# Performance work log

Hardware: AMD Instinct MI355X
Metric: run time of the kernel (lower is better)

Reference implementation:

```python
import jax, jax.numpy as jnp
import numpy as np

B, S, H, M, E = 64, 512, 1024, 26, 676  # batch, seq, hidden, max_nodes, max_edges (M*M)


def setup_inputs() -> dict:
    key = jax.random.key(0)
    ks = jax.random.split(key, 16)
    seq = jax.random.normal(ks[0], (B, S, H), jnp.float32)
    # ragged, strictly-increasing sentence-end offsets in [1, S-1], zero-padded tail
    rng = np.random.RandomState(0)
    off = np.zeros((B, M - 1), np.int64)
    for b in range(B):
        c = rng.randint(5, M)  # count of valid offsets per sample (ragged)
        off[b, :c] = np.sort(rng.choice(np.arange(1, S), size=c, replace=False))
    s = 1.0 / np.sqrt(H)
    s3 = 1.0 / np.sqrt(3 * H)
    return {
        'sequence_outputs': seq,
        'proof_offsets': jnp.asarray(off),
        'node_labels': jax.random.randint(ks[1], (B, M), 0, 2),
        'edge_labels': jax.random.randint(ks[2], (B, E), 0, 2),
        'W_naf': jax.random.normal(ks[3], (H, H), jnp.float32) * s,
        'b_naf': jnp.zeros((H,), jnp.float32),
        'W_cd': jax.random.normal(ks[4], (H, H), jnp.float32) * s,
        'b_cd': jnp.zeros((H,), jnp.float32),
        'W_co': jax.random.normal(ks[5], (H, 2), jnp.float32) * s,
        'b_co': jnp.zeros((2,), jnp.float32),
        'W_nd': jax.random.normal(ks[6], (H, H), jnp.float32) * s,
        'b_nd': jnp.zeros((H,), jnp.float32),
        'W_no': jax.random.normal(ks[7], (H, 2), jnp.float32) * s,
        'b_no': jnp.zeros((2,), jnp.float32),
        'W_ed': jax.random.normal(ks[8], (3 * H, H), jnp.float32) * s3,
        'b_ed': jnp.zeros((H,), jnp.float32),
        'W_eo': jax.random.normal(ks[9], (H, 2), jnp.float32) * s,
        'b_eo': jnp.zeros((2,), jnp.float32),
    }


def reference(sequence_outputs, proof_offsets, node_labels, edge_labels,
              W_naf, b_naf, W_cd, b_cd, W_co, b_co,
              W_nd, b_nd, W_no, b_no, W_ed, b_ed, W_eo, b_eo):
    Bx, Sx, Hx = sequence_outputs.shape
    Mx = node_labels.shape[1]
    Ex = edge_labels.shape[1]

    cls = sequence_outputs[:, 0, :]                       # [B,H]
    naf = cls @ W_naf + b_naf                             # NAF node embedding
    logits = jnp.tanh(cls @ W_cd + b_cd) @ W_co + b_co    # RobertaClassificationHead (eval: dropout=id)

    # segment-mean pooling via inclusive prefix sums: segment j = tokens (prev_j, off_j]
    P = jnp.cumsum(sequence_outputs, axis=1)              # [B,S,H]
    off = proof_offsets                                   # [B,M-1]
    prev = jnp.concatenate([jnp.zeros((Bx, 1), off.dtype), off[:, :-1]], axis=1)
    valid = off > 0                                       # [B,M-1]
    seg_sum = (jnp.take_along_axis(P, off[..., None], axis=1)
               - jnp.take_along_axis(P, prev[..., None], axis=1))  # [B,M-1,H]
    seg_len = jnp.maximum(off - prev, 1).astype(sequence_outputs.dtype)
    seg_mean = seg_sum / seg_len[..., None] * valid[..., None]

    count = valid.sum(axis=1)                             # nodes per sample (excl. NAF)
    # node embeddings: seg means at 0..count-1, NAF at index count, zeros after
    node_full = jnp.concatenate([seg_mean, jnp.zeros((Bx, 1, Hx), seg_mean.dtype)], axis=1)  # [B,M,H]
    idx = jnp.arange(Mx)
    node_full = node_full + (idx[None, :, None] == count[:, None, None]) * naf[:, None, :]

    # all-pairs edge features over n=count+1 nodes, row-major flat k=i*n+j, zero-padded to E
    n = count + 1                                         # [B]
    k = jnp.arange(Ex)                                    # [E]
    i = jnp.clip(k[None, :] // n[:, None], 0, Mx - 1)     # [B,E]
    j = jnp.clip(k[None, :] % n[:, None], 0, Mx - 1)
    valid_e = (k[None, :] < (n * n)[:, None])[..., None]
    ni = jnp.take_along_axis(node_full, i[..., None], axis=1)  # [B,E,H]
    nj = jnp.take_along_axis(node_full, j[..., None], axis=1)
    edge = jnp.concatenate([nj, ni, nj - ni], axis=-1) * valid_e  # [B,E,3H]

    node_logits = jnp.tanh(node_full @ W_nd + b_nd) @ W_no + b_no
    edge_logits = jnp.tanh(edge @ W_ed + b_ed) @ W_eo + b_eo
    return (logits, node_logits, edge_logits)
```

## Files before the change

### kernel.cpp

```cpp
#include <hip/hip_runtime.h>
#include <hip/hip_bf16.h>

#define B_ 64
#define S_ 512
#define H_ 1024
#define M_ 26
#define E_ 676

typedef short bf16x8 __attribute__((ext_vector_type(8)));
typedef float f32x4 __attribute__((ext_vector_type(4)));

__device__ __forceinline__ void gload16(const void* g, void* l) {
    __builtin_amdgcn_global_load_lds((const __attribute__((address_space(1))) unsigned int*)g,
                                     (__attribute__((address_space(3))) unsigned int*)l,
                                     16, 0, 0);
}

__device__ __forceinline__ float tanh_fast(float x) {
    float e = __expf(2.0f * x);
    return 1.0f - 2.0f * __builtin_amdgcn_rcpf(e + 1.0f);
}

__global__ __launch_bounds__(256) void k_stage1(
    const float* __restrict__ seq, const int* __restrict__ off,
    const float* __restrict__ Wnaf, const float* __restrict__ Wcd,
    const float* __restrict__ Wnd, const float* __restrict__ Wed,
    const float* __restrict__ bed, const float* __restrict__ Weo,
    const float* __restrict__ beo,
    __hip_bfloat16* __restrict__ Wt, int* __restrict__ count,
    float* __restrict__ econ, float* __restrict__ naf, float* __restrict__ cdh,
    float* __restrict__ node_sum) {
    __shared__ float smem[2048];
    int bid = blockIdx.x;
    int tid = threadIdx.x;

    if (bid < 3072) {
        float (*T)[33] = (float(*)[33])smem;
        int s = bid >> 10, rem = bid & 1023;
        int bx = rem & 31, by = rem >> 5;
        int c = tid & 31, r0 = tid >> 5;
        const int HH = H_ * H_;
#pragma unroll
        for (int i = 0; i < 4; ++i) {
            int r = r0 + 8 * i;
            size_t k = by * 32 + r, n = bx * 32 + c;
            float v;
            if (s == 0)      v = Wnd[k * H_ + n];
            else if (s == 1) v = Wed[k * H_ + n] + Wed[2 * HH + k * H_ + n];
            else             v = Wed[HH + k * H_ + n] - Wed[2 * HH + k * H_ + n];
            T[r][c] = v;
        }
        __syncthreads();
#pragma unroll
        for (int i = 0; i < 4; ++i) {
            int rr = r0 + 8 * i;
            Wt[(size_t)(s * H_ + bx * 32 + rr) * H_ + by * 32 + c] = __float2bfloat16(T[c][rr]);
        }
    } else if (bid == 3072) {
        if (tid < 64) {
            int b = tid;
            int c = 0;
            for (int m = 0; m < M_ - 1; ++m) c += (off[b * (M_ - 1) + m] > 0) ? 1 : 0;
            count[b] = c;
        }
    } else if (bid == 3073) {
        float* s0 = smem; float* s1 = smem + 256;
        float a0 = 0.f, a1 = 0.f;
        for (int h = tid; h < H_; h += 256) {
            float t = tanh_fast(bed[h]);
            a0 += t * Weo[h * 2 + 0];
            a1 += t * Weo[h * 2 + 1];
        }
        s0[tid] = a0; s1[tid] = a1; __syncthreads();
        for (int o = 128; o > 0; o >>= 1) {
            if (tid < o) { s0[tid] += s0[tid + o]; s1[tid] += s1[tid + o]; }
            __syncthreads();
        }
        if (tid == 0) { econ[0] = s0[0] + beo[0]; econ[1] = s1[0] + beo[1]; }
    } else if (bid < 3330) {
        float (*As)[64] = (float(*)[64])smem;
        float (*Bs)[64] = (float(*)[64])(smem + 1024);
        int e = bid - 3074;
        int bx = e & 31;
        int kbase = (e >> 5) * 128;
        const float* W;
        float* dst;
        int cbase;
        if (bx < 16) { W = Wnaf; dst = naf; cbase = bx * 64; }
        else         { W = Wcd;  dst = cdh; cbase = (bx - 16) * 64; }
        int tx = tid % 16, ty = tid / 16;
        float c[4][4] = {};
        int la_row = tid / 4;
        int la_k4  = (tid % 4) * 4;
        int lb_k   = tid / 16;
        int lb_c4  = (tid % 16) * 4;
        for (int k0 = 0; k0 < 128; k0 += 16) {
            float4 a = *(const float4*)(seq + (size_t)la_row * S_ * H_ + kbase + k0 + la_k4);
            *(float4*)(&Bs[lb_k][lb_c4]) =
                *(const float4*)(W + (size_t)(kbase + k0 + lb_k) * H_ + cbase + lb_c4);
            As[la_k4 + 0][la_row] = a.x;
            As[la_k4 + 1][la_row] = a.y;
            As[la_k4 + 2][la_row] = a.z;
            As[la_k4 + 3][la_row] = a.w;
            __syncthreads();
#pragma unroll
            for (int kk = 0; kk < 16; ++kk) {
                float4 av = *(const float4*)(&As[kk][ty * 4]);
                float4 bv = *(const float4*)(&Bs[kk][tx * 4]);
                c[0][0] += av.x * bv.x; c[0][1] += av.x * bv.y; c[0][2] += av.x * bv.z; c[0][3] += av.x * bv.w;
                c[1][0] += av.y * bv.x; c[1][1] += av.y * bv.y; c[1][2] += av.y * bv.z; c[1][3] += av.y * bv.w;
                c[2][0] += av.z * bv.x; c[2][1] += av.z * bv.y; c[2][2] += av.z * bv.z; c[2][3] += av.z * bv.w;
                c[3][0] += av.w * bv.x; c[3][1] += av.w * bv.y; c[3][2] += av.w * bv.z; c[3][3] += av.w * bv.w;
            }
            __syncthreads();
        }
#pragma unroll
        for (int i = 0; i < 4; ++i)
#pragma unroll
            for (int j = 0; j < 4; ++j)
                atomicAdd(dst + (size_t)(ty * 4 + i) * H_ + cbase + tx * 4 + j, c[i][j]);
    } else {
        int e = bid - 3330;
        int chunk = e & 15, b = e >> 4;
        int* offs = (int*)smem;
        int* cs = (int*)smem + 28;
        if (tid < M_ - 1) offs[tid] = off[b * (M_ - 1) + tid];
        __syncthreads();
        if (tid == 0) {
            int c = 0;
            while (c < M_ - 1 && offs[c] > 0) c++;
            cs[0] = c; cs[1] = (c > 0) ? offs[c - 1] : 0;
        }
        __syncthreads();
        int c = cs[0], offmax = cs[1];
        int t0 = chunk * 32;
        int ts = max(t0, 1), te = min(t0 + 31, offmax);
        if (ts > te) return;
        int m = 0;
        while (m < c && offs[m] < ts) m++;
        const float4* sq = (const float4*)(seq + (size_t)b * S_ * H_);
        float4 acc = make_float4(0, 0, 0, 0);
        for (int t = ts; t <= te; ++t) {
            if (offs[m] < t) {
                float* dst = node_sum + ((size_t)(b * M_ + m)) * H_ + tid * 4;
                atomicAdd(dst + 0, acc.x); atomicAdd(dst + 1, acc.y);
                atomicAdd(dst + 2, acc.z); atomicAdd(dst + 3, acc.w);
                acc = make_float4(0, 0, 0, 0);
                while (offs[m] < t) m++;
            }
            float4 v = sq[(size_t)t * (H_ / 4) + tid];
            acc.x += v.x; acc.y += v.y; acc.z += v.z; acc.w += v.w;
        }
        float* dst = node_sum + ((size_t)(b * M_ + m)) * H_ + tid * 4;
        atomicAdd(dst + 0, acc.x); atomicAdd(dst + 1, acc.y);
        atomicAdd(dst + 2, acc.z); atomicAdd(dst + 3, acc.w);
    }
}

__global__ __launch_bounds__(256) void k_stage2(
    const float* __restrict__ sums, const int* __restrict__ off,
    const int* __restrict__ count, const float* __restrict__ naf,
    const float* __restrict__ bnaf, __hip_bfloat16* __restrict__ nodeB,
    const float* __restrict__ cdh, const float* __restrict__ bcd,
    const float* __restrict__ Wco, const float* __restrict__ bco,
    float* __restrict__ out) {
    __shared__ float smem[512];
    int bid = blockIdx.x;
    int tid = threadIdx.x;
    if (bid < 1664) {
        int b = bid / 26, m = bid - b * 26;
        int cnt = count[b];
        float4 v = make_float4(0, 0, 0, 0);
        const float4* row = (const float4*)(sums + ((size_t)(b * M_ + m)) * H_);
        if (m < M_ - 1) {
            int o = off[b * (M_ - 1) + m];
            if (o > 0) {
                int prev = (m > 0) ? off[b * (M_ - 1) + m - 1] : 0;
                float inv = 1.0f / (float)max(o - prev, 1);
                float4 s = row[tid];
                v = make_float4(s.x * inv, s.y * inv, s.z * inv, s.w * inv);
            }
        }
        if (m == cnt) {
            float4 a = ((const float4*)(naf + (size_t)b * H_))[tid];
            float4 bb = ((const float4*)bnaf)[tid];
            v.x += a.x + bb.x; v.y += a.y + bb.y; v.z += a.z + bb.z; v.w += a.w + bb.w;
        }
        __hip_bfloat16 __attribute__((aligned(8))) h[4] = {
            __float2bfloat16(v.x), __float2bfloat16(v.y),
            __float2bfloat16(v.z), __float2bfloat16(v.w)};
        *(ushort4*)(nodeB + ((size_t)(b * M_ + m)) * H_ + tid * 4) = *(const ushort4*)h;
    } else {
        int b = bid - 1664;
        float* s0 = smem; float* s1 = smem + 256;
        float a0 = 0.f, a1 = 0.f;
        for (int h = tid; h < H_; h += 256) {
            float t = tanh_fast(cdh[(size_t)b * H_ + h] + bcd[h]);
            a0 += t * Wco[h * 2 + 0];
            a1 += t * Wco[h * 2 + 1];
        }
        s0[tid] = a0; s1[tid] = a1; __syncthreads();
        for (int o = 128; o > 0; o >>= 1) {
            if (tid < o) { s0[tid] += s0[tid + o]; s1[tid] += s1[tid + o]; }
            __syncthreads();
        }
        if (tid == 0) { out[b * 2 + 0] = s0[0] + bco[0]; out[b * 2 + 1] = s1[0] + bco[1]; }
    }
}

#define GM 1664
#define GN 3072
#define GK 1024
__global__ __launch_bounds__(256) void k_mfma(const __hip_bfloat16* __restrict__ A,
                                              const __hip_bfloat16* __restrict__ Bt,
                                              float* __restrict__ C) {
    __shared__ __hip_bfloat16 As[128 * 32];
    __shared__ __hip_bfloat16 Bs[128 * 32];
    int tid = threadIdx.x;
    int wid = tid >> 6, ln = tid & 63;
    int row0 = blockIdx.y * 128, col0 = blockIdx.x * 128;
    const __hip_bfloat16* ga = A + (size_t)(row0 + wid * 16 + (ln >> 2)) * GK + (ln & 3) * 8;
    const __hip_bfloat16* gb = Bt + (size_t)(col0 + wid * 16 + (ln >> 2)) * GK + (ln & 3) * 8;
    __hip_bfloat16* lA = As + wid * 512;
    __hip_bfloat16* lB = Bs + wid * 512;
    int mrow = (wid >> 1) * 64, ncol = (wid & 1) * 64;
    int l15 = ln & 15, l4 = ln >> 4;
    f32x4 acc[4][4] = {};
    const __hip_bfloat16* pa = As + (size_t)(mrow + l15) * 32 + l4 * 8;
    const __hip_bfloat16* pb = Bs + (size_t)(ncol + l15) * 32 + l4 * 8;
    for (int k0 = 0; k0 < GK; k0 += 32) {
        gload16(ga, lA);
        gload16(ga + 64 * GK, lA + 2048);
        gload16(gb, lB);
        gload16(gb + 64 * GK, lB + 2048);
        ga += 32; gb += 32;
        __syncthreads();
        bf16x8 af[4], bf[4];
#pragma unroll
        for (int mi = 0; mi < 4; ++mi) af[mi] = *(const bf16x8*)(pa + mi * 16 * 32);
#pragma unroll
        for (int ni = 0; ni < 4; ++ni) bf[ni] = *(const bf16x8*)(pb + ni * 16 * 32);
#pragma unroll
        for (int mi = 0; mi < 4; ++mi)
#pragma unroll
            for (int ni = 0; ni < 4; ++ni)
                acc[mi][ni] = __builtin_amdgcn_mfma_f32_16x16x32_bf16(af[mi], bf[ni],
                                                                      acc[mi][ni], 0, 0, 0);
        __syncthreads();
    }
#pragma unroll
    for (int mi = 0; mi < 4; ++mi)
#pragma unroll
        for (int ni = 0; ni < 4; ++ni) {
            f32x4 v = acc[mi][ni];
            size_t r = row0 + mrow + mi * 16 + l4 * 4;
            size_t cc = col0 + ncol + ni * 16 + l15;
            C[(r + 0) * GN + cc] = v[0];
            C[(r + 1) * GN + cc] = v[1];
            C[(r + 2) * GN + cc] = v[2];
            C[(r + 3) * GN + cc] = v[3];
        }
}

__global__ __launch_bounds__(256) void k_stage4(
    const float* __restrict__ Cm, const int* __restrict__ count,
    const float* __restrict__ bnd, const float* __restrict__ Wno,
    const float* __restrict__ bno, const float* __restrict__ bed,
    const float* __restrict__ Weo, const float* __restrict__ beo,
    const float* __restrict__ econ, float* __restrict__ out_n,
    float* __restrict__ out_e) {
    int bid = blockIdx.x;
    int wid = threadIdx.x >> 6, lane = threadIdx.x & 63;
    if (bid < 416) {
        int r = bid * 4 + wid;
        const float4* src = (const float4*)(Cm + (size_t)r * GN);
        float a0 = 0.f, a1 = 0.f;
#pragma unroll
        for (int it = 0; it < 4; ++it) {
            int h = lane * 4 + it * 256;
            float4 s = src[lane + it * 64];
            float4 bb = *(const float4*)(bnd + h);
            float t0 = tanh_fast(s.x + bb.x), t1 = tanh_fast(s.y + bb.y);
            float t2 = tanh_fast(s.z + bb.z), t3 = tanh_fast(s.w + bb.w);
            a0 += t0 * Wno[h * 2 + 0] + t1 * Wno[h * 2 + 2] + t2 * Wno[h * 2 + 4] + t3 * Wno[h * 2 + 6];
            a1 += t0 * Wno[h * 2 + 1] + t1 * Wno[h * 2 + 3] + t2 * Wno[h * 2 + 5] + t3 * Wno[h * 2 + 7];
        }
        for (int o = 32; o > 0; o >>= 1) { a0 += __shfl_down(a0, o); a1 += __shfl_down(a1, o); }
        if (lane == 0) { out_n[(size_t)r * 2 + 0] = a0 + bno[0]; out_n[(size_t)r * 2 + 1] = a1 + bno[1]; }
    } else {
        int e = bid - 416;
        int b = e >> 4;
        int wg = (e & 15) * 4 + wid;
        int n = count[b] + 1;
        int n2 = n * n;
        float4 bed4[4], w04[4], w14[4];
#pragma unroll
        for (int it = 0; it < 4; ++it) {
            int h = lane * 4 + it * 256;
            bed4[it] = *(const float4*)(bed + h);
            w04[it] = make_float4(Weo[h * 2 + 0], Weo[h * 2 + 2], Weo[h * 2 + 4], Weo[h * 2 + 6]);
            w14[it] = make_float4(Weo[h * 2 + 1], Weo[h * 2 + 3], Weo[h * 2 + 5], Weo[h * 2 + 7]);
        }
        float e0 = econ[0], e1 = econ[1];
        float b0 = beo[0], b1 = beo[1];
        for (int k = wg; k < E_; k += 64) {
            float* dst = out_e + ((size_t)b * E_ + k) * 2;
            if (k >= n2) {
                if (lane == 0) { dst[0] = e0; dst[1] = e1; }
                continue;
            }
            int i = k / n, j = k - i * n;
            const float4* U4 = (const float4*)(Cm + (size_t)(b * M_ + j) * GN + H_);
            const float4* V4 = (const float4*)(Cm + (size_t)(b * M_ + i) * GN + 2 * H_);
            float a0 = 0.f, a1 = 0.f;
#pragma unroll
            for (int it = 0; it < 4; ++it) {
                float4 u = U4[lane + it * 64];
                float4 v = V4[lane + it * 64];
                float t0 = tanh_fast(u.x + v.x + bed4[it].x);
                float t1 = tanh_fast(u.y + v.y + bed4[it].y);
                float t2 = tanh_fast(u.z + v.z + bed4[it].z);
                float t3 = tanh_fast(u.w + v.w + bed4[it].w);
                a0 += t0 * w04[it].x + t1 * w04[it].y + t2 * w04[it].z + t3 * w04[it].w;
                a1 += t0 * w14[it].x + t1 * w14[it].y + t2 * w14[it].z + t3 * w14[it].w;
            }
            for (int o = 32; o > 0; o >>= 1) { a0 += __shfl_down(a0, o); a1 += __shfl_down(a1, o); }
            if (lane == 0) { dst[0] = a0 + b0; dst[1] = a1 + b1; }
        }
    }
}

extern "C" void kernel_launch(void* const* d_in, const int* in_sizes, int n_in,
                              void* d_out, int out_size, void* d_ws, size_t ws_size,
                              hipStream_t stream) {
    const float* seq  = (const float*)d_in[0];
    const int*   off  = (const int*)d_in[1];
    const float* Wnaf = (const float*)d_in[4];  const float* bnaf = (const float*)d_in[5];
    const float* Wcd  = (const float*)d_in[6];  const float* bcd  = (const float*)d_in[7];
    const float* Wco  = (const float*)d_in[8];  const float* bco  = (const float*)d_in[9];
    const float* Wnd  = (const float*)d_in[10]; const float* bnd  = (const float*)d_in[11];
    const float* Wno  = (const float*)d_in[12]; const float* bno  = (const float*)d_in[13];
    const float* Wed  = (const float*)d_in[14]; const float* bed  = (const float*)d_in[15];
    const float* Weo  = (const float*)d_in[16]; const float* beo  = (const float*)d_in[17];
    float* out = (float*)d_out;

    float* ws = (float*)d_ws;
    size_t p = 0;
    float* nodeS = ws + p;  p += (size_t)B_ * M_ * H_;
    float* naf   = ws + p;  p += (size_t)B_ * H_;
    float* cdh   = ws + p;  p += (size_t)B_ * H_;
    __hip_bfloat16* nodeB = (__hip_bfloat16*)(ws + p); p += (size_t)B_ * M_ * H_ / 2;
    __hip_bfloat16* Wt    = (__hip_bfloat16*)(ws + p); p += (size_t)3 * H_ * H_ / 2;
    float* Cbuf  = ws + p;  p += (size_t)B_ * M_ * 3 * H_;
    int*   cnt   = (int*)(ws + p); p += 64;
    float* econ  = ws + p;  p += 2;

    hipMemsetAsync(nodeS, 0, ((size_t)B_ * M_ * H_ + 2 * (size_t)B_ * H_) * sizeof(float),
                   stream);

    k_stage1<<<dim3(4354), 256, 0, stream>>>(seq, off, Wnaf, Wcd, Wnd, Wed, bed, Weo, beo,
                                             Wt, cnt, econ, naf, cdh, nodeS);
    k_stage2<<<dim3(1728), 256, 0, stream>>>(nodeS, off, cnt, naf, bnaf, nodeB,
                                             cdh, bcd, Wco, bco, out);
    k_mfma<<<dim3(GN / 128, GM / 128), 256, 0, stream>>>(nodeB, Wt, Cbuf);
    k_stage4<<<dim3(1440), 256, 0, stream>>>(Cbuf, cnt, bnd, Wno, bno, bed, Weo, beo, econ,
                                             out + B_ * 2, out + B_ * 2 + B_ * M_ * 2);
}
```

Measured before the change: 311.1 us.

## Software-pipeline segment sum loads and reorder stage1 block roles

The segment-sum blocks now each cover 64 tokens instead of 32 and move to the front of the grid. They double-buffer eight-row float4 register batches so loads overlap with accumulation and atomic flushes. Block order is rearranged so the long seq-streaming work starts first, with the weight transposes after the GEMV blocks and count/econ at the end. The cost is higher register pressure and fewer segment blocks. The removed c>0 guard and the new m<M_ check change edge handling.

```diff
diff --git a/kernel.cpp b/kernel.cpp
--- a/kernel.cpp
+++ b/kernel.cpp
@@ -19,6 +19,27 @@
 __device__ __forceinline__ float tanh_fast(float x) {
     float e = __expf(2.0f * x);
     return 1.0f - 2.0f * __builtin_amdgcn_rcpf(e + 1.0f);
+}
+
+__device__ __forceinline__ void seg_load(float4 (&R)[8], const float* sq, int tb) {
+#pragma unroll
+    for (int i = 0; i < 8; ++i) R[i] = *(const float4*)(sq + (size_t)(tb + i) * H_);
+}
+__device__ __forceinline__ void seg_cons(const float4 (&R)[8], int tb, float4& acc,
+                                         int& m, int& cur, int c, const int* offs,
+                                         float* base) {
+#pragma unroll
+    for (int i = 0; i < 8; ++i) {
+        acc.x += R[i].x; acc.y += R[i].y; acc.z += R[i].z; acc.w += R[i].w;
+        if (tb + i == cur) {
+            float* d = base + (size_t)m * H_;
+            atomicAdd(d + 0, acc.x); atomicAdd(d + 1, acc.y);
+            atomicAdd(d + 2, acc.z); atomicAdd(d + 3, acc.w);
+            acc = make_float4(0.f, 0.f, 0.f, 0.f);
+            ++m;
+            cur = (m < c) ? offs[m] : 0x7fffffff;
+        }
+    }
 }
 
 __global__ __launch_bounds__(256) void k_stage1(
@@ -34,53 +55,77 @@
     int bid = blockIdx.x;
     int tid = threadIdx.x;
 
-    if (bid < 3072) {
-        float (*T)[33] = (float(*)[33])smem;
-        int s = bid >> 10, rem = bid & 1023;
-        int bx = rem & 31, by = rem >> 5;
-        int c = tid & 31, r0 = tid >> 5;
-        const int HH = H_ * H_;
-#pragma unroll
-        for (int i = 0; i < 4; ++i) {
-            int r = r0 + 8 * i;
-            size_t k = by * 32 + r, n = bx * 32 + c;
-            float v;
-            if (s == 0)      v = Wnd[k * H_ + n];
-            else if (s == 1) v = Wed[k * H_ + n] + Wed[2 * HH + k * H_ + n];
-            else             v = Wed[HH + k * H_ + n] - Wed[2 * HH + k * H_ + n];
-            T[r][c] = v;
-        }
+    if (bid < 512) {
+        int b = bid >> 3, kk = bid & 7;
+        int* offs = (int*)smem;
+        int* cs = (int*)smem + 28;
+        if (tid < M_ - 1) offs[tid] = off[b * (M_ - 1) + tid];
         __syncthreads();
-#pragma unroll
-        for (int i = 0; i < 4; ++i) {
-            int rr = r0 + 8 * i;
-            Wt[(size_t)(s * H_ + bx * 32 + rr) * H_ + by * 32 + c] = __float2bfloat16(T[c][rr]);
-        }
-    } else if (bid == 3072) {
-        if (tid < 64) {
-            int b = tid;
+        if (tid == 0) {
             int c = 0;
-            for (int m = 0; m < M_ - 1; ++m) c += (off[b * (M_ - 1) + m] > 0) ? 1 : 0;
-            count[b] = c;
-        }
-    } else if (bid == 3073) {
-        float* s0 = smem; float* s1 = smem + 256;
-        float a0 = 0.f, a1 = 0.f;
-        for (int h = tid; h < H_; h += 256) {
-            float t = tanh_fast(bed[h]);
-            a0 += t * Weo[h * 2 + 0];
-            a1 += t * Weo[h * 2 + 1];
-        }
-        s0[tid] = a0; s1[tid] = a1; __syncthreads();
-        for (int o = 128; o > 0; o >>= 1) {
-            if (tid < o) { s0[tid] += s0[tid + o]; s1[tid] += s1[tid + o]; }
-            __syncthreads();
-        }
-        if (tid == 0) { econ[0] = s0[0] + beo[0]; econ[1] = s1[0] + beo[1]; }
-    } else if (bid < 3330) {
+            while (c < M_ - 1 && offs[c] > 0) c++;
+            cs[0] = c; cs[1] = offs[c - 1];
+        }
+        __syncthreads();
+        int c = cs[0], offmax = cs[1];
+        int t0 = kk * 64;
+        int ts = (t0 < 1) ? 1 : t0;
+        int te = (t0 + 63 < offmax) ? t0 + 63 : offmax;
+        if (ts > te) return;
+        int m = 0;
+        while (m < c && offs[m] < ts) m++;
+        int cur = (m < c) ? offs[m] : 0x7fffffff;
+        const float* sq = seq + (size_t)b * S_ * H_ + tid * 4;
+        float* base = node_sum + (size_t)b * M_ * H_ + tid * 4;
+        float4 acc = make_float4(0.f, 0.f, 0.f, 0.f);
+        int t = ts;
+        float4 A[8], Bv[8];
+        if (t + 7 <= te) seg_load(A, sq, t);
+        while (t + 7 <= te) {
+            if (t + 15 <= te) seg_load(Bv, sq, t + 8);
+            __builtin_amdgcn_sched_barrier(0);
+            seg_cons(A, t, acc, m, cur, c, offs, base);
+            t += 8;
+            if (!(t + 7 <= te)) break;
+            if (t + 15 <= te) seg_load(A, sq, t + 8);
+            __builtin_amdgcn_sched_barrier(0);
+            seg_cons(Bv, t, acc, m, cur, c, offs, base);
+            t += 8;
+        }
+        int rem = te - t + 1;
+        if (rem > 0) {
+            float4 Tl[7];
+#pragma unroll
+            for (int i = 0; i < 7; ++i) {
+                int tt = (i < rem) ? t + i : ts;
+                Tl[i] = *(const float4*)(sq + (size_t)tt * H_);
+            }
+            __builtin_amdgcn_sched_barrier(0);
+#pragma unroll
+            for (int i = 0; i < 7; ++i) {
+                if (i < rem) {
+                    acc.x += Tl[i].x; acc.y += Tl[i].y;
+                    acc.z += Tl[i].z; acc.w += Tl[i].w;
+                    if (t + i == cur) {
+                        float* d = base + (size_t)m * H_;
+                        atomicAdd(d + 0, acc.x); atomicAdd(d + 1, acc.y);
+                        atomicAdd(d + 2, acc.z); atomicAdd(d + 3, acc.w);
+                        acc = make_float4(0.f, 0.f, 0.f, 0.f);
+                        ++m;
+                        cur = (m < c) ? offs[m] : 0x7fffffff;
+                    }
+                }
+            }
+        }
+        if (m < M_) {
+            float* d = base + (size_t)m * H_;
+            atomicAdd(d + 0, acc.x); atomicAdd(d + 1, acc.y);
+            atomicAdd(d + 2, acc.z); atomicAdd(d + 3, acc.w);
+        }
+    } else if (bid < 768) {
         float (*As)[64] = (float(*)[64])smem;
         float (*Bs)[64] = (float(*)[64])(smem + 1024);
-        int e = bid - 3074;
+        int e = bid - 512;
         int bx = e & 31;
         int kbase = (e >> 5) * 128;
         const float* W;
@@ -119,41 +164,50 @@
 #pragma unroll
             for (int j = 0; j < 4; ++j)
                 atomicAdd(dst + (size_t)(ty * 4 + i) * H_ + cbase + tx * 4 + j, c[i][j]);
+    } else if (bid < 3840) {
+        float (*T)[33] = (float(*)[33])smem;
+        int idx = bid - 768;
+        int s = idx >> 10, rem = idx & 1023;
+        int bx = rem & 31, by = rem >> 5;
+        int c = tid & 31, r0 = tid >> 5;
+        const int HH = H_ * H_;
+#pragma unroll
+        for (int i = 0; i < 4; ++i) {
+            int r = r0 + 8 * i;
+            size_t k = by * 32 + r, n = bx * 32 + c;
+            float v;
+            if (s == 0)      v = Wnd[k * H_ + n];
+            else if (s == 1) v = Wed[k * H_ + n] + Wed[2 * HH + k * H_ + n];
+            else             v = Wed[HH + k * H_ + n] - Wed[2 * HH + k * H_ + n];
+            T[r][c] = v;
+        }
+        __syncthreads();
+#pragma unroll
+        for (int i = 0; i < 4; ++i) {
+            int rr = r0 + 8 * i;
+            Wt[(size_t)(s * H_ + bx * 32 + rr) * H_ + by * 32 + c] = __float2bfloat16(T[c][rr]);
+        }
+    } else if (bid == 3840) {
+        if (tid < 64) {
+            int b = tid;
+            int c = 0;
+            for (int m = 0; m < M_ - 1; ++m) c += (off[b * (M_ - 1) + m] > 0) ? 1 : 0;
+            count[b] = c;
+        }
     } else {
-        int e = bid - 3330;
-        int chunk = e & 15, b = e >> 4;
-        int* offs = (int*)smem;
-        int* cs = (int*)smem + 28;
-        if (tid < M_ - 1) offs[tid] = off[b * (M_ - 1) + tid];
-        __syncthreads();
-        if (tid == 0) {
-            int c = 0;
-            while (c < M_ - 1 && offs[c] > 0) c++;
-            cs[0] = c; cs[1] = (c > 0) ? offs[c - 1] : 0;
-        }
-        __syncthreads();
-        int c = cs[0], offmax = cs[1];
-        int t0 = chunk * 32;
-        int ts = max(t0, 1), te = min(t0 + 31, offmax);
-        if (ts > te) return;
-        int m = 0;
-        while (m < c && offs[m] < ts) m++;
-        const float4* sq = (const float4*)(seq + (size_t)b * S_ * H_);
-        float4 acc = make_float4(0, 0, 0, 0);
-        for (int t = ts; t <= te; ++t) {
-            if (offs[m] < t) {
-                float* dst = node_sum + ((size_t)(b * M_ + m)) * H_ + tid * 4;
-                atomicAdd(dst + 0, acc.x); atomicAdd(dst + 1, acc.y);
-                atomicAdd(dst + 2, acc.z); atomicAdd(dst + 3, acc.w);
-                acc = make_float4(0, 0, 0, 0);
-                while (offs[m] < t) m++;
-            }
-            float4 v = sq[(size_t)t * (H_ / 4) + tid];
-            acc.x += v.x; acc.y += v.y; acc.z += v.z; acc.w += v.w;
-        }
-        float* dst = node_sum + ((size_t)(b * M_ + m)) * H_ + tid * 4;
-        atomicAdd(dst + 0, acc.x); atomicAdd(dst + 1, acc.y);
-        atomicAdd(dst + 2, acc.z); atomicAdd(dst + 3, acc.w);
+        float* s0 = smem; float* s1 = smem + 256;
+        float a0 = 0.f, a1 = 0.f;
+        for (int h = tid; h < H_; h += 256) {
+            float t = tanh_fast(bed[h]);
+            a0 += t * Weo[h * 2 + 0];
+            a1 += t * Weo[h * 2 + 1];
+        }
+        s0[tid] = a0; s1[tid] = a1; __syncthreads();
+        for (int o = 128; o > 0; o >>= 1) {
+            if (tid < o) { s0[tid] += s0[tid + o]; s1[tid] += s1[tid + o]; }
+            __syncthreads();
+        }
+        if (tid == 0) { econ[0] = s0[0] + beo[0]; econ[1] = s1[0] + beo[1]; }
     }
 }
 
@@ -358,7 +412,7 @@
     hipMemsetAsync(nodeS, 0, ((size_t)B_ * M_ * H_ + 2 * (size_t)B_ * H_) * sizeof(float),
                    stream);
 
-    k_stage1<<<dim3(4354), 256, 0, stream>>>(seq, off, Wnaf, Wcd, Wnd, Wed, bed, Weo, beo,
+    k_stage1<<<dim3(3842), 256, 0, stream>>>(seq, off, Wnaf, Wcd, Wnd, Wed, bed, Weo, beo,
                                              Wt, cnt, econ, naf, cdh, nodeS);
     k_stage2<<<dim3(1728), 256, 0, stream>>>(nodeS, off, cnt, naf, bnaf, nodeB,
                                              cdh, bcd, Wco, bco, out);
```

Result: no change. 307.9 us (-1.0%).
